# Kernel optimization log

Hardware: AMD Instinct MI355X
Metric: run time of the kernel (lower is better)

The kernel has to match this reference:

```python
import jax, jax.numpy as jnp
import numpy as np

N = 100000
E = 1600000
F_IN = 128
HID = 128
C = 10
NEG_SLOPE = 0.2


def setup_inputs() -> dict:
    key = jax.random.key(0)
    ks = jax.random.split(key, 12)
    x = jax.random.normal(ks[0], (N, F_IN), dtype=jnp.float32)
    edge_index = jax.random.randint(ks[1], (2, E), 0, N, dtype=jnp.int64)
    batch = jnp.zeros((N,), dtype=jnp.int64)
    s1 = 1.0 / np.sqrt(F_IN)
    s2 = 1.0 / np.sqrt(HID)
    return {
        "x": x,
        "edge_index": edge_index,
        "batch": batch,
        "W1": jax.random.normal(ks[2], (F_IN, HID), dtype=jnp.float32) * s1,
        "a_src1": jax.random.normal(ks[3], (HID,), dtype=jnp.float32) * s2,
        "a_dst1": jax.random.normal(ks[4], (HID,), dtype=jnp.float32) * s2,
        "b1": jnp.zeros((HID,), dtype=jnp.float32),
        "W2": jax.random.normal(ks[5], (HID, HID), dtype=jnp.float32) * s2,
        "a_src2": jax.random.normal(ks[6], (HID,), dtype=jnp.float32) * s2,
        "a_dst2": jax.random.normal(ks[7], (HID,), dtype=jnp.float32) * s2,
        "b2": jnp.zeros((HID,), dtype=jnp.float32),
        "Wlin": jax.random.normal(ks[8], (HID, C), dtype=jnp.float32) * s2,
        "blin": jnp.zeros((C,), dtype=jnp.float32),
    }


def gat_conv(x, src, dst, W, a_src, a_dst, b):
    # PyG GATConv, heads=1: h = xW; alpha_e = softmax_dst(leaky_relu(a_src.h[src] + a_dst.h[dst]))
    h = x @ W                                  # [N, H]
    alpha_s = h @ a_src                        # [N]
    alpha_d = h @ a_dst                        # [N]
    e = jax.nn.leaky_relu(alpha_s[src] + alpha_d[dst], NEG_SLOPE)  # [E]
    m = jax.ops.segment_max(e, dst, num_segments=N)                # per-dst max (stable softmax)
    ex = jnp.exp(e - m[dst])
    denom = jax.ops.segment_sum(ex, dst, num_segments=N)
    alpha = ex / (denom[dst] + 1e-16)          # [E]
    out = jax.ops.segment_sum(h[src] * alpha[:, None], dst, num_segments=N)
    return out + b


def reference(x, edge_index, batch, W1, a_src1, a_dst1, b1, W2, a_src2, a_dst2, b2, Wlin, blin):
    x = x.astype(jnp.float32)
    loops = jnp.arange(N, dtype=edge_index.dtype)
    src = jnp.concatenate([edge_index[0], loops])  # add_self_loops=True
    dst = jnp.concatenate([edge_index[1], loops])
    h = jax.nn.relu(gat_conv(x, src, dst, W1, a_src1, a_dst1, b1))
    h = jax.nn.relu(gat_conv(h, src, dst, W2, a_src2, a_dst2, b2))
    # dropout(p=0.5) is identity in eval mode
    return h @ Wlin + blin
```

## Files before the change

### kernel.cpp

```cpp
#include <hip/hip_runtime.h>

#define N_NODES 100000
#define N_EDGES 1600000
#define TOTE    (N_EDGES + N_NODES)
#define NEG     0.2f
#define NB      ((N_NODES + 255) >> 8)
#define BCAP    5120
#define BINBLK  391

typedef __attribute__((ext_vector_type(8))) short bf16x8;
typedef __attribute__((ext_vector_type(4))) float floatx4;

__device__ __forceinline__ unsigned short f2bf(float f) {
  unsigned int u = __float_as_uint(f);
  u += 0x7fffu + ((u >> 16) & 1u);
  return (unsigned short)(u >> 16);
}
__device__ __forceinline__ float bf_lo(unsigned int r) { return __uint_as_float(r << 16); }
__device__ __forceinline__ float bf_hi(unsigned int r) { return __uint_as_float(r & 0xffff0000u); }

__global__ __launch_bounds__(256) void k_wprep(const float* __restrict__ W1, const float* __restrict__ W2,
                                               unsigned short* __restrict__ B1hi, unsigned short* __restrict__ B1lo,
                                               unsigned short* __restrict__ B2hi, unsigned short* __restrict__ B2lo,
                                               int* __restrict__ bucketCnt) {
  int b = blockIdx.x;
  int t = threadIdx.x;
  if (b == 16) {
    for (int i = t; i < NB * 16; i += 256) bucketCnt[i] = 0;
    return;
  }
  const float* W = (b < 8) ? W1 : W2;
  unsigned short* Bh = (b < 8) ? B1hi : B2hi;
  unsigned short* Bl = (b < 8) ? B1lo : B2lo;
  int ntile = b & 7;
  int kq = t >> 6, lane = t & 63;
  int q = lane >> 4, m = lane & 15;
  int n = ntile * 16 + m;
  union { unsigned short us[8]; uint4 u4; } hi, lo;
#pragma unroll
  for (int j = 0; j < 8; ++j) {
    int k = kq * 32 + q * 8 + j;
    float w = W[(size_t)k * 128 + n];
    unsigned int u = __float_as_uint(w);
    hi.us[j] = (unsigned short)(u >> 16);
    float res = w - __uint_as_float(u & 0xffff0000u);
    lo.us[j] = f2bf(res);
  }
  size_t fo = ((size_t)(ntile * 4 + kq) * 64 + lane) * 8;
  *reinterpret_cast<uint4*>(Bh + fo) = hi.u4;
  *reinterpret_cast<uint4*>(Bl + fo) = lo.u4;
}

__global__ __launch_bounds__(256, 4) void k_binA_gemm1(
    const int* __restrict__ ei, int* __restrict__ bucketCnt, unsigned int* __restrict__ binned,
    const float* __restrict__ x,
    const unsigned short* __restrict__ Bhi, const unsigned short* __restrict__ Blo,
    unsigned short* __restrict__ Cb,
    const float* __restrict__ avS, const float* __restrict__ avD,
    float* __restrict__ aS, float* __restrict__ aD,
    float* __restrict__ slotS, float* __restrict__ slotD) {
  __shared__ union {
    struct { int hist[NB]; int cur[NB]; } a;
    struct { char sbuf[64 * 528]; float redS[256]; float redD[256];
             float mS[64]; float mD[64]; } g;
  } sm;
  int t = threadIdx.x;

  if (blockIdx.x < BINBLK) {
    for (int b = t; b < NB; b += 256) sm.a.hist[b] = 0;
    __syncthreads();
    unsigned int pk[16]; int bk[16];
#pragma unroll
    for (int j = 0; j < 16; ++j) {
      int idx = blockIdx.x * 4096 + j * 256 + t;
      if (idx < N_EDGES) {
        int s = ei[idx], d = ei[N_EDGES + idx];
        bk[j] = d >> 8;
        pk[j] = ((unsigned int)s << 8) | (unsigned int)(d & 255);
        atomicAdd(&sm.a.hist[bk[j]], 1);
      } else bk[j] = -1;
    }
    __syncthreads();
    for (int b = t; b < NB; b += 256) {
      int h = sm.a.hist[b];
      if (h) sm.a.cur[b] = b * BCAP + atomicAdd(&bucketCnt[b * 16], h);
    }
    __syncthreads();
#pragma unroll
    for (int j = 0; j < 16; ++j) {
      if (bk[j] >= 0) {
        int pos = atomicAdd(&sm.a.cur[bk[j]], 1);
        binned[pos] = pk[j];
      }
    }
    return;
  }

  int bid = blockIdx.x - BINBLK;
  int w = t >> 6, lane = t & 63;
  int q = lane >> 4, m = lane & 15;
  int rbase = bid * 64;
  const char* Ab = (const char*)x;

  for (int c = w; c < 33; c += 4) {
    int L = c * 1024 + lane * 16;
    int r = L / 528;
    int off = L - r * 528;
    int gr = min(rbase + r, N_NODES - 1);
    const char* src = (off < 512) ? (Ab + (size_t)gr * 512 + off) : Ab;
    __builtin_amdgcn_global_load_lds((const __attribute__((address_space(1))) void*)src,
                                     (__attribute__((address_space(3))) void*)(sm.g.sbuf + c * 1024),
                                     16, 0, 0);
  }

  floatx4 acc[4][2];
#pragma unroll
  for (int mt = 0; mt < 4; ++mt)
#pragma unroll
    for (int nt = 0; nt < 2; ++nt) acc[mt][nt] = (floatx4){0.f, 0.f, 0.f, 0.f};

  __syncthreads();

#pragma unroll
  for (int k0 = 0; k0 < 4; ++k0) {
    bf16x8 Bh[2], Bl[2], Ah[4], Al[4];
#pragma unroll
    for (int nt = 0; nt < 2; ++nt) {
      int ntg = w * 2 + nt;
      size_t fo = ((size_t)(ntg * 4 + k0) * 64 + lane) * 8;
      Bh[nt] = *reinterpret_cast<const bf16x8*>(Bhi + fo);
      Bl[nt] = *reinterpret_cast<const bf16x8*>(Blo + fo);
    }
#pragma unroll
    for (int mt = 0; mt < 4; ++mt) {
      int R = mt * 16 + m;
      const char* ap = sm.g.sbuf + R * 528 + k0 * 128 + q * 32;
      float4 v0 = *reinterpret_cast<const float4*>(ap);
      float4 v1 = *reinterpret_cast<const float4*>(ap + 16);
      float av[8] = {v0.x, v0.y, v0.z, v0.w, v1.x, v1.y, v1.z, v1.w};
      union { unsigned short us[8]; bf16x8 v; } uh, ul;
#pragma unroll
      for (int j = 0; j < 8; ++j) {
        unsigned int u = __float_as_uint(av[j]);
        uh.us[j] = (unsigned short)(u >> 16);
        float res = av[j] - __uint_as_float(u & 0xffff0000u);
        ul.us[j] = f2bf(res);
      }
      Ah[mt] = uh.v; Al[mt] = ul.v;
    }
#pragma unroll
    for (int mt = 0; mt < 4; ++mt)
#pragma unroll
      for (int nt = 0; nt < 2; ++nt) {
        acc[mt][nt] = __builtin_amdgcn_mfma_f32_16x16x32_bf16(Ah[mt], Bh[nt], acc[mt][nt], 0, 0, 0);
        acc[mt][nt] = __builtin_amdgcn_mfma_f32_16x16x32_bf16(Ah[mt], Bl[nt], acc[mt][nt], 0, 0, 0);
        acc[mt][nt] = __builtin_amdgcn_mfma_f32_16x16x32_bf16(Al[mt], Bh[nt], acc[mt][nt], 0, 0, 0);
      }
  }

  float avs[2], avd[2];
#pragma unroll
  for (int nt = 0; nt < 2; ++nt) {
    int c = w * 32 + nt * 16 + m;
    avs[nt] = avS[c];
    avd[nt] = avD[c];
  }
#pragma unroll
  for (int mt = 0; mt < 4; ++mt)
#pragma unroll
    for (int r = 0; r < 4; ++r) {
      float ps = acc[mt][0][r] * avs[0] + acc[mt][1][r] * avs[1];
      float pd = acc[mt][0][r] * avd[0] + acc[mt][1][r] * avd[1];
      ps += __shfl_xor(ps, 1); pd += __shfl_xor(pd, 1);
      ps += __shfl_xor(ps, 2); pd += __shfl_xor(pd, 2);
      ps += __shfl_xor(ps, 4); pd += __shfl_xor(pd, 4);
      ps += __shfl_xor(ps, 8); pd += __shfl_xor(pd, 8);
      if (m == 0) {
        int rl = mt * 16 + q * 4 + r;
        sm.g.redS[rl * 4 + w] = ps;
        sm.g.redD[rl * 4 + w] = pd;
      }
    }

  __syncthreads();
  unsigned short* sC = (unsigned short*)sm.g.sbuf;

#pragma unroll
  for (int mt = 0; mt < 4; ++mt)
#pragma unroll
    for (int nt = 0; nt < 2; ++nt)
#pragma unroll
      for (int r = 0; r < 4; ++r) {
        int rl = mt * 16 + q * 4 + r;
        int cl = w * 32 + nt * 16 + m;
        sC[rl * 136 + cl] = f2bf(acc[mt][nt][r]);
      }
  __syncthreads();

#pragma unroll
  for (int i = 0; i < 4; ++i) {
    int idx = i * 256 + t;
    int rl = idx >> 4, kk = idx & 15;
    int gr = rbase + rl;
    if (gr < N_NODES)
      *reinterpret_cast<uint4*>(Cb + (size_t)gr * 128 + kk * 8) =
          *reinterpret_cast<const uint4*>(sC + rl * 136 + kk * 8);
  }

  if (t < 64) {
    int gr = rbase + t;
    bool ok = gr < N_NODES;
    float ps = sm.g.redS[t * 4] + sm.g.redS[t * 4 + 1] + sm.g.redS[t * 4 + 2] + sm.g.redS[t * 4 + 3];
    float pd = sm.g.redD[t * 4] + sm.g.redD[t * 4 + 1] + sm.g.redD[t * 4 + 2] + sm.g.redD[t * 4 + 3];
    if (ok) { aS[gr] = ps; aD[gr] = pd; }
    sm.g.mS[t] = ok ? ps : -1e30f;
    sm.g.mD[t] = ok ? pd : -1e30f;
  }
  __syncthreads();
#pragma unroll
  for (int off = 32; off > 0; off >>= 1) {
    if (t < off) {
      sm.g.mS[t] = fmaxf(sm.g.mS[t], sm.g.mS[t + off]);
      sm.g.mD[t] = fmaxf(sm.g.mD[t], sm.g.mD[t + off]);
    }
    __syncthreads();
  }
  if (t == 0) { slotS[bid] = sm.g.mS[0]; slotD[bid] = sm.g.mD[0]; }
}

__global__ __launch_bounds__(512) void k_bin_scan(const int* __restrict__ bucketCnt,
                                                  int* __restrict__ binOffs) {
  __shared__ int sc[512];
  int t = threadIdx.x;
  int v = (t < NB) ? bucketCnt[t * 16] : 0;
  sc[t] = v; __syncthreads();
  for (int off = 1; off < 512; off <<= 1) {
    int x = (t >= off) ? sc[t - off] : 0;
    __syncthreads();
    sc[t] += x;
    __syncthreads();
  }
  int excl = sc[t] - v;
  if (t <= NB) binOffs[t] = excl;
}

__global__ __launch_bounds__(256) void k_binB(const unsigned int* __restrict__ binned,
                                              const int* __restrict__ binOffs,
                                              int* __restrict__ offs, int* __restrict__ srcs) {
  __shared__ int cnt[256];
  __shared__ int sc[256];
  __shared__ int cur[256];
  int b = blockIdx.x;
  int t = threadIdx.x;
  int node0 = b << 8;
  int nNodes = min(256, N_NODES - node0);
  int cntE = binOffs[b + 1] - binOffs[b];
  int e0 = b * BCAP, e1 = e0 + cntE;
  int base = binOffs[b] + node0;

  cnt[t] = 0; __syncthreads();
  for (int i = e0 + t; i < e1; i += 256) atomicAdd(&cnt[binned[i] & 255u], 1);
  __syncthreads();

  int v = (t < nNodes) ? cnt[t] + 1 : 0;
  sc[t] = v; __syncthreads();
  for (int off = 1; off < 256; off <<= 1) {
    int x = (t >= off) ? sc[t - off] : 0;
    __syncthreads();
    sc[t] += x;
    __syncthreads();
  }
  int excl = sc[t] - v;
  if (t < nNodes) {
    offs[node0 + t] = base + excl;
    srcs[base + excl] = node0 + t;
  }
  cur[t] = excl + 1;
  __syncthreads();

  for (int i = e0 + t; i < e1; i += 256) {
    unsigned int e = binned[i];
    int j = (int)(e & 255u);
    int s = (int)(e >> 8);
    int p = atomicAdd(&cur[j], 1);
    srcs[base + p] = s;
  }
  if (b == 0 && t == 0) offs[N_NODES] = TOTE;
}

template <bool SPLIT>
__global__ __launch_bounds__(256, 4) void k_gemm_mfma(const void* __restrict__ Aptr,
                                                   const unsigned short* __restrict__ Bhi,
                                                   const unsigned short* __restrict__ Blo,
                                                   unsigned short* __restrict__ Cb,
                                                   const float* __restrict__ avS, const float* __restrict__ avD,
                                                   float* __restrict__ aS, float* __restrict__ aD,
                                                   float* __restrict__ slotS, float* __restrict__ slotD) {
  constexpr int SRCB  = SPLIT ? 512 : 256;
  constexpr int ROWB  = SPLIT ? 528 : 272;
  constexpr int ABYTES = 64 * ROWB;
  constexpr int CHUNKS = ABYTES / 1024;
  __shared__ char sbuf[ABYTES];
  __shared__ float redS[64 * 4], redD[64 * 4];
  __shared__ float mS[64], mD[64];
  int t = threadIdx.x;
  int w = t >> 6, lane = t & 63;
  int q = lane >> 4, m = lane & 15;
  int rbase = blockIdx.x * 64;
  const char* Ab = (const char*)Aptr;

  for (int c = w; c < CHUNKS; c += 4) {
    int L = c * 1024 + lane * 16;
    int r = L / ROWB;
    int off = L - r * ROWB;
    int gr = min(rbase + r, N_NODES - 1);
    const char* src = (off < SRCB) ? (Ab + (size_t)gr * SRCB + off) : Ab;
    __builtin_amdgcn_global_load_lds((const __attribute__((address_space(1))) void*)src,
                                     (__attribute__((address_space(3))) void*)(sbuf + c * 1024),
                                     16, 0, 0);
  }

  floatx4 acc[4][2];
#pragma unroll
  for (int mt = 0; mt < 4; ++mt)
#pragma unroll
    for (int nt = 0; nt < 2; ++nt) acc[mt][nt] = (floatx4){0.f, 0.f, 0.f, 0.f};

  __syncthreads();

#pragma unroll
  for (int k0 = 0; k0 < 4; ++k0) {
    bf16x8 Bh[2], Bl[2], Ah[4], Al[4];
#pragma unroll
    for (int nt = 0; nt < 2; ++nt) {
      int ntg = w * 2 + nt;
      size_t fo = ((size_t)(ntg * 4 + k0) * 64 + lane) * 8;
      Bh[nt] = *reinterpret_cast<const bf16x8*>(Bhi + fo);
      Bl[nt] = *reinterpret_cast<const bf16x8*>(Blo + fo);
    }
#pragma unroll
    for (int mt = 0; mt < 4; ++mt) {
      int R = mt * 16 + m;
      if constexpr (SPLIT) {
        const char* ap = sbuf + R * ROWB + k0 * 128 + q * 32;
        float4 v0 = *reinterpret_cast<const float4*>(ap);
        float4 v1 = *reinterpret_cast<const float4*>(ap + 16);
        float av[8] = {v0.x, v0.y, v0.z, v0.w, v1.x, v1.y, v1.z, v1.w};
        union { unsigned short us[8]; bf16x8 v; } uh, ul;
#pragma unroll
        for (int j = 0; j < 8; ++j) {
          unsigned int u = __float_as_uint(av[j]);
          uh.us[j] = (unsigned short)(u >> 16);
          float res = av[j] - __uint_as_float(u & 0xffff0000u);
          ul.us[j] = f2bf(res);
        }
        Ah[mt] = uh.v; Al[mt] = ul.v;
      } else {
        Ah[mt] = *reinterpret_cast<const bf16x8*>(sbuf + R * ROWB + k0 * 64 + q * 16);
      }
    }
#pragma unroll
    for (int mt = 0; mt < 4; ++mt)
#pragma unroll
      for (int nt = 0; nt < 2; ++nt) {
        acc[mt][nt] = __builtin_amdgcn_mfma_f32_16x16x32_bf16(Ah[mt], Bh[nt], acc[mt][nt], 0, 0, 0);
        acc[mt][nt] = __builtin_amdgcn_mfma_f32_16x16x32_bf16(Ah[mt], Bl[nt], acc[mt][nt], 0, 0, 0);
        if constexpr (SPLIT)
          acc[mt][nt] = __builtin_amdgcn_mfma_f32_16x16x32_bf16(Al[mt], Bh[nt], acc[mt][nt], 0, 0, 0);
      }
  }

  float avs[2], avd[2];
#pragma unroll
  for (int nt = 0; nt < 2; ++nt) {
    int c = w * 32 + nt * 16 + m;
    avs[nt] = avS[c];
    avd[nt] = avD[c];
  }
#pragma unroll
  for (int mt = 0; mt < 4; ++mt)
#pragma unroll
    for (int r = 0; r < 4; ++r) {
      float ps = acc[mt][0][r] * avs[0] + acc[mt][1][r] * avs[1];
      float pd = acc[mt][0][r] * avd[0] + acc[mt][1][r] * avd[1];
      ps += __shfl_xor(ps, 1); pd += __shfl_xor(pd, 1);
      ps += __shfl_xor(ps, 2); pd += __shfl_xor(pd, 2);
      ps += __shfl_xor(ps, 4); pd += __shfl_xor(pd, 4);
      ps += __shfl_xor(ps, 8); pd += __shfl_xor(pd, 8);
      if (m == 0) {
        int rl = mt * 16 + q * 4 + r;
        redS[rl * 4 + w] = ps;
        redD[rl * 4 + w] = pd;
      }
    }

  __syncthreads();
  unsigned short* sC = (unsigned short*)sbuf;

#pragma unroll
  for (int mt = 0; mt < 4; ++mt)
#pragma unroll
    for (int nt = 0; nt < 2; ++nt)
#pragma unroll
      for (int r = 0; r < 4; ++r) {
        int rl = mt * 16 + q * 4 + r;
        int cl = w * 32 + nt * 16 + m;
        sC[rl * 136 + cl] = f2bf(acc[mt][nt][r]);
      }
  __syncthreads();

#pragma unroll
  for (int i = 0; i < 4; ++i) {
    int idx = i * 256 + t;
    int rl = idx >> 4, kk = idx & 15;
    int gr = rbase + rl;
    if (gr < N_NODES)
      *reinterpret_cast<uint4*>(Cb + (size_t)gr * 128 + kk * 8) =
          *reinterpret_cast<const uint4*>(sC + rl * 136 + kk * 8);
  }

  if (t < 64) {
    int gr = rbase + t;
    bool ok = gr < N_NODES;
    float ps = redS[t * 4] + redS[t * 4 + 1] + redS[t * 4 + 2] + redS[t * 4 + 3];
    float pd = redD[t * 4] + redD[t * 4 + 1] + redD[t * 4 + 2] + redD[t * 4 + 3];
    if (ok) { aS[gr] = ps; aD[gr] = pd; }
    mS[t] = ok ? ps : -1e30f;
    mD[t] = ok ? pd : -1e30f;
  }
  __syncthreads();
#pragma unroll
  for (int off = 32; off > 0; off >>= 1) {
    if (t < off) { mS[t] = fmaxf(mS[t], mS[t + off]); mD[t] = fmaxf(mD[t], mD[t + off]); }
    __syncthreads();
  }
  if (t == 0) { slotS[blockIdx.x] = mS[0]; slotD[blockIdx.x] = mD[0]; }
}

__global__ __launch_bounds__(256) void k_gmax(const float* __restrict__ slotS,
                                              const float* __restrict__ slotD,
                                              int n, float* __restrict__ gMh) {
  __shared__ float sS[256], sD[256];
  int t = threadIdx.x;
  float ms = -1e30f, md = -1e30f;
  for (int i = t; i < n; i += 256) { ms = fmaxf(ms, slotS[i]); md = fmaxf(md, slotD[i]); }
  sS[t] = ms; sD[t] = md;
  __syncthreads();
#pragma unroll
  for (int off = 128; off > 0; off >>= 1) {
    if (t < off) { sS[t] = fmaxf(sS[t], sS[t + off]); sD[t] = fmaxf(sD[t], sD[t + off]); }
    __syncthreads();
  }
  if (t == 0) {
    float M = sS[0] + sD[0];
    gMh[0] = (M > 0.f) ? M : NEG * M;
  }
}

#define FMA8(E, R)                                     \
  do {                                                 \
    acc[0] += (E) * bf_lo((R).x); acc[1] += (E) * bf_hi((R).x); \
    acc[2] += (E) * bf_lo((R).y); acc[3] += (E) * bf_hi((R).y); \
    acc[4] += (E) * bf_lo((R).z); acc[5] += (E) * bf_hi((R).z); \
    acc[6] += (E) * bf_lo((R).w); acc[7] += (E) * bf_hi((R).w); \
  } while (0)

#define LDG(R0, R1, R2, R3, E0, E1, E2, E3, J)                                                   \
  do {                                                                                           \
    float2 q0 = pairs[pbase + (J) + 0];                                                          \
    float2 q1 = pairs[pbase + (J) + 1];                                                          \
    float2 q2 = pairs[pbase + (J) + 2];                                                          \
    float2 q3 = pairs[pbase + (J) + 3];                                                          \
    E0 = q0.x; E1 = q1.x; E2 = q2.x; E3 = q3.x;                                                  \
    R0 = *reinterpret_cast<const uint4*>(hbl + ((size_t)(unsigned)__float_as_int(q0.y) << 7));   \
    R1 = *reinterpret_cast<const uint4*>(hbl + ((size_t)(unsigned)__float_as_int(q1.y) << 7));   \
    R2 = *reinterpret_cast<const uint4*>(hbl + ((size_t)(unsigned)__float_as_int(q2.y) << 7));   \
    R3 = *reinterpret_cast<const uint4*>(hbl + ((size_t)(unsigned)__float_as_int(q3.y) << 7));   \
  } while (0)
#define FMAG(R0, R1, R2, R3, E0, E1, E2, E3) \
  do { FMA8(E0, R0); FMA8(E1, R1); FMA8(E2, R2); FMA8(E3, R3); } while (0)

template <bool FINAL>
__global__ __launch_bounds__(256) void k_aggregate(const unsigned short* __restrict__ hb,
                                                   const float* __restrict__ aS,
                                                   const float* __restrict__ aD,
                                                   const int* __restrict__ offs,
                                                   const int* __restrict__ srcs,
                                                   const float* __restrict__ bias,
                                                   const float* __restrict__ gMh,
                                                   unsigned short* __restrict__ outb,
                                                   const float* __restrict__ Wl,
                                                   const float* __restrict__ bl,
                                                   float* __restrict__ out) {
  __shared__ float2 pairs[16 * 17];
  __shared__ float sWt[FINAL ? 10 * 144 : 1];
  __shared__ float sbl[FINAL ? 16 : 1];
  int t = threadIdx.x;
  if constexpr (FINAL) {
    if (t < 128) {
      int jj = t >> 5, ii = t & 31;
#pragma unroll
      for (int c = 0; c < 10; ++c) sWt[c * 144 + jj * 36 + ii] = Wl[t * 10 + c];
    }
    if (t < 10) sbl[t] = bl[t];
    __syncthreads();
  }
  int g = t >> 4;
  int l = t & 15;
  int dst = blockIdx.x * 16 + g;
  float Mh = gMh[0];
  int beg = offs[dst], end = offs[dst + 1];
  float adn = aD[dst];
  float denom = 0.f;
  float acc[8];
#pragma unroll
  for (int k = 0; k < 8; ++k) acc[k] = 0.f;
  const int pbase = g * 17;
  const unsigned short* hbl = hb + l * 8;

  uint4 ra0, ra1, ra2, ra3, rb0, rb1, rb2, rb3;
  float ea0, ea1, ea2, ea3, eb0, eb1, eb2, eb3;

  for (int chunk = beg; chunk < end; chunk += 16) {
    int i = chunk + l;
    float ex = 0.f; int s = 0;
    if (i < end) {
      s = srcs[i];
      float e = aS[s] + adn;
      e = (e > 0.f) ? e : NEG * e;
      ex = __expf(e - Mh);
    }
    denom += ex;
    pairs[pbase + l] = make_float2(ex, __int_as_float(s));
    int cnt = end - chunk; if (cnt > 16) cnt = 16;
    LDG(ra0, ra1, ra2, ra3, ea0, ea1, ea2, ea3, 0);
    int j = 0;
    for (;;) {
      bool more = (j + 4) < cnt;
      if (more) LDG(rb0, rb1, rb2, rb3, eb0, eb1, eb2, eb3, j + 4);
      FMAG(ra0, ra1, ra2, ra3, ea0, ea1, ea2, ea3);
      j += 4;
      if (!more) break;
      bool more2 = (j + 4) < cnt;
      if (more2) LDG(ra0, ra1, ra2, ra3, ea0, ea1, ea2, ea3, j + 4);
      FMAG(rb0, rb1, rb2, rb3, eb0, eb1, eb2, eb3);
      j += 4;
      if (!more2) break;
    }
  }

  denom += __shfl_xor(denom, 1);
  denom += __shfl_xor(denom, 2);
  denom += __shfl_xor(denom, 4);
  denom += __shfl_xor(denom, 8);
  float inv = 1.f / (denom + 1e-16f);
  float4 b0 = *reinterpret_cast<const float4*>(bias + l * 8);
  float4 b1 = *reinterpret_cast<const float4*>(bias + l * 8 + 4);
  float o0 = fmaxf(acc[0] * inv + b0.x, 0.f), o1 = fmaxf(acc[1] * inv + b0.y, 0.f);
  float o2 = fmaxf(acc[2] * inv + b0.z, 0.f), o3 = fmaxf(acc[3] * inv + b0.w, 0.f);
  float o4 = fmaxf(acc[4] * inv + b1.x, 0.f), o5 = fmaxf(acc[5] * inv + b1.y, 0.f);
  float o6 = fmaxf(acc[6] * inv + b1.z, 0.f), o7 = fmaxf(acc[7] * inv + b1.w, 0.f);

  if constexpr (!FINAL) {
    union { unsigned short us[8]; uint4 u4; } oo;
    oo.us[0] = f2bf(o0); oo.us[1] = f2bf(o1); oo.us[2] = f2bf(o2); oo.us[3] = f2bf(o3);
    oo.us[4] = f2bf(o4); oo.us[5] = f2bf(o5); oo.us[6] = f2bf(o6); oo.us[7] = f2bf(o7);
    *reinterpret_cast<uint4*>(outb + (size_t)dst * 128 + l * 8) = oo.u4;
  } else {
    float p[10];
#pragma unroll
    for (int c = 0; c < 10; ++c) {
      const float4* wp = reinterpret_cast<const float4*>(&sWt[c * 144 + (l >> 2) * 36 + (l & 3) * 8]);
      float4 w0 = wp[0], w1 = wp[1];
      p[c] = o0 * w0.x + o1 * w0.y + o2 * w0.z + o3 * w0.w +
             o4 * w1.x + o5 * w1.y + o6 * w1.z + o7 * w1.w;
    }
#pragma unroll
    for (int c = 0; c < 10; ++c) {
      p[c] += __shfl_xor(p[c], 1);
      p[c] += __shfl_xor(p[c], 2);
      p[c] += __shfl_xor(p[c], 4);
      p[c] += __shfl_xor(p[c], 8);
    }
    if (l == 0) {
      float* orow = out + (size_t)dst * 10;
      *reinterpret_cast<float2*>(orow + 0) = make_float2(p[0] + sbl[0], p[1] + sbl[1]);
      *reinterpret_cast<float2*>(orow + 2) = make_float2(p[2] + sbl[2], p[3] + sbl[3]);
      *reinterpret_cast<float2*>(orow + 4) = make_float2(p[4] + sbl[4], p[5] + sbl[5]);
      *reinterpret_cast<float2*>(orow + 6) = make_float2(p[6] + sbl[6], p[7] + sbl[7]);
      *reinterpret_cast<float2*>(orow + 8) = make_float2(p[8] + sbl[8], p[9] + sbl[9]);
    }
  }
}

extern "C" void kernel_launch(void* const* d_in, const int* in_sizes, int n_in,
                              void* d_out, int out_size, void* d_ws, size_t ws_size,
                              hipStream_t stream) {
  const float* x   = (const float*)d_in[0];
  const int*   ei  = (const int*)d_in[1];
  const float* W1  = (const float*)d_in[3];
  const float* as1 = (const float*)d_in[4];
  const float* ad1 = (const float*)d_in[5];
  const float* b1  = (const float*)d_in[6];
  const float* W2  = (const float*)d_in[7];
  const float* as2 = (const float*)d_in[8];
  const float* ad2 = (const float*)d_in[9];
  const float* b2  = (const float*)d_in[10];
  const float* Wl  = (const float*)d_in[11];
  const float* bl  = (const float*)d_in[12];
  float* out = (float*)d_out;

  char* p = (char*)d_ws;
  unsigned short* hb   = (unsigned short*)p; p += (size_t)N_NODES * 128 * sizeof(unsigned short);
  unsigned short* hagg = (unsigned short*)p; p += (size_t)N_NODES * 128 * sizeof(unsigned short);
  float* aS    = (float*)p; p += (size_t)N_NODES * sizeof(float);
  float* aD    = (float*)p; p += (size_t)N_NODES * sizeof(float);
  int* offs    = (int*)p;   p += (size_t)(N_NODES + 4) * sizeof(int);
  int* srcs    = (int*)p;   p += (size_t)TOTE * sizeof(int);
  int* bucketCnt = (int*)p; p += (size_t)NB * 16 * sizeof(int);
  int* binOffs   = (int*)p; p += (size_t)(NB + 4) * sizeof(int);
  float* slotS = (float*)p; p += 2048 * sizeof(float);
  float* slotD = (float*)p; p += 2048 * sizeof(float);
  float* gMh = (float*)p;   p += 4 * sizeof(float);
  unsigned short* B1hi = (unsigned short*)p; p += 128 * 128 * sizeof(unsigned short);
  unsigned short* B1lo = (unsigned short*)p; p += 128 * 128 * sizeof(unsigned short);
  unsigned short* B2hi = (unsigned short*)p; p += 128 * 128 * sizeof(unsigned short);
  unsigned short* B2lo = (unsigned short*)p; p += 128 * 128 * sizeof(unsigned short);
  unsigned int* binned = (unsigned int*)hagg;

  int gemmBlocks = (N_NODES + 63) / 64;
  int aggBlocks  = N_NODES / 16;

  k_wprep<<<17, 256, 0, stream>>>(W1, W2, B1hi, B1lo, B2hi, B2lo, bucketCnt);
  k_binA_gemm1<<<BINBLK + gemmBlocks, 256, 0, stream>>>(ei, bucketCnt, binned,
                                                        x, B1hi, B1lo, hb, as1, ad1,
                                                        aS, aD, slotS, slotD);
  k_bin_scan<<<1, 512, 0, stream>>>(bucketCnt, binOffs);
  k_binB<<<NB, 256, 0, stream>>>(binned, binOffs, offs, srcs);
  k_gmax<<<1, 256, 0, stream>>>(slotS, slotD, gemmBlocks, gMh);
  k_aggregate<false><<<aggBlocks, 256, 0, stream>>>(hb, aS, aD, offs, srcs, b1, gMh, hagg,
                                                    nullptr, nullptr, nullptr);
  k_gemm_mfma<false><<<gemmBlocks, 256, 0, stream>>>(hagg, B2hi, B2lo, hb, as2, ad2, aS, aD, slotS, slotD);
  k_gmax<<<1, 256, 0, stream>>>(slotS, slotD, gemmBlocks, gMh);
  k_aggregate<true><<<aggBlocks, 256, 0, stream>>>(hb, aS, aD, offs, srcs, b2, gMh, hagg,
                                                   Wl, bl, out);
}
```

Measured before the change: 325.1 us.

## Split layer-1 GEMM across both binning kernels to overlap with bin phases

The first-layer feature GEMM blocks are split in half. One half still runs alongside the edge-binning pass A, and the other half now runs inside a new fused kernel alongside binning pass B, which replaces the standalone k_binB. This balances work between the two launches so GEMM blocks fill the GPU while the latency-bound binning blocks run. The cost is a larger shared-memory footprint for the binning blocks in pass B, which shares a union with the GEMM buffers and may lower occupancy.

```diff
diff --git a/kernel.cpp b/kernel.cpp
--- a/kernel.cpp
+++ b/kernel.cpp
@@ -7,6 +7,8 @@
 #define NB      ((N_NODES + 255) >> 8)
 #define BCAP    5120
 #define BINBLK  391
+#define G1H1    782
+#define G1H2    781
 
 typedef __attribute__((ext_vector_type(8))) short bf16x8;
 typedef __attribute__((ext_vector_type(4))) float floatx4;
@@ -49,6 +51,142 @@
   size_t fo = ((size_t)(ntile * 4 + kq) * 64 + lane) * 8;
   *reinterpret_cast<uint4*>(Bh + fo) = hi.u4;
   *reinterpret_cast<uint4*>(Bl + fo) = lo.u4;
+}
+
+__device__ __forceinline__ void gemm1_body(
+    int bid, int t, char* sbuf, float* redS, float* redD, float* mS, float* mD,
+    const float* __restrict__ x,
+    const unsigned short* __restrict__ Bhi, const unsigned short* __restrict__ Blo,
+    unsigned short* __restrict__ Cb,
+    const float* __restrict__ avS, const float* __restrict__ avD,
+    float* __restrict__ aS, float* __restrict__ aD,
+    float* __restrict__ slotS, float* __restrict__ slotD) {
+  int w = t >> 6, lane = t & 63;
+  int q = lane >> 4, m = lane & 15;
+  int rbase = bid * 64;
+  const char* Ab = (const char*)x;
+
+  for (int c = w; c < 33; c += 4) {
+    int L = c * 1024 + lane * 16;
+    int r = L / 528;
+    int off = L - r * 528;
+    int gr = min(rbase + r, N_NODES - 1);
+    const char* src = (off < 512) ? (Ab + (size_t)gr * 512 + off) : Ab;
+    __builtin_amdgcn_global_load_lds((const __attribute__((address_space(1))) void*)src,
+                                     (__attribute__((address_space(3))) void*)(sbuf + c * 1024),
+                                     16, 0, 0);
+  }
+
+  floatx4 acc[4][2];
+#pragma unroll
+  for (int mt = 0; mt < 4; ++mt)
+#pragma unroll
+    for (int nt = 0; nt < 2; ++nt) acc[mt][nt] = (floatx4){0.f, 0.f, 0.f, 0.f};
+
+  __syncthreads();
+
+#pragma unroll
+  for (int k0 = 0; k0 < 4; ++k0) {
+    bf16x8 Bh[2], Bl[2], Ah[4], Al[4];
+#pragma unroll
+    for (int nt = 0; nt < 2; ++nt) {
+      int ntg = w * 2 + nt;
+      size_t fo = ((size_t)(ntg * 4 + k0) * 64 + lane) * 8;
+      Bh[nt] = *reinterpret_cast<const bf16x8*>(Bhi + fo);
+      Bl[nt] = *reinterpret_cast<const bf16x8*>(Blo + fo);
+    }
+#pragma unroll
+    for (int mt = 0; mt < 4; ++mt) {
+      int R = mt * 16 + m;
+      const char* ap = sbuf + R * 528 + k0 * 128 + q * 32;
+      float4 v0 = *reinterpret_cast<const float4*>(ap);
+      float4 v1 = *reinterpret_cast<const float4*>(ap + 16);
+      float av[8] = {v0.x, v0.y, v0.z, v0.w, v1.x, v1.y, v1.z, v1.w};
+      union { unsigned short us[8]; bf16x8 v; } uh, ul;
+#pragma unroll
+      for (int j = 0; j < 8; ++j) {
+        unsigned int u = __float_as_uint(av[j]);
+        uh.us[j] = (unsigned short)(u >> 16);
+        float res = av[j] - __uint_as_float(u & 0xffff0000u);
+        ul.us[j] = f2bf(res);
+      }
+      Ah[mt] = uh.v; Al[mt] = ul.v;
+    }
+#pragma unroll
+    for (int mt = 0; mt < 4; ++mt)
+#pragma unroll
+      for (int nt = 0; nt < 2; ++nt) {
+        acc[mt][nt] = __builtin_amdgcn_mfma_f32_16x16x32_bf16(Ah[mt], Bh[nt], acc[mt][nt], 0, 0, 0);
+        acc[mt][nt] = __builtin_amdgcn_mfma_f32_16x16x32_bf16(Ah[mt], Bl[nt], acc[mt][nt], 0, 0, 0);
+        acc[mt][nt] = __builtin_amdgcn_mfma_f32_16x16x32_bf16(Al[mt], Bh[nt], acc[mt][nt], 0, 0, 0);
+      }
+  }
+
+  float avs[2], avd[2];
+#pragma unroll
+  for (int nt = 0; nt < 2; ++nt) {
+    int c = w * 32 + nt * 16 + m;
+    avs[nt] = avS[c];
+    avd[nt] = avD[c];
+  }
+#pragma unroll
+  for (int mt = 0; mt < 4; ++mt)
+#pragma unroll
+    for (int r = 0; r < 4; ++r) {
+      float ps = acc[mt][0][r] * avs[0] + acc[mt][1][r] * avs[1];
+      float pd = acc[mt][0][r] * avd[0] + acc[mt][1][r] * avd[1];
+      ps += __shfl_xor(ps, 1); pd += __shfl_xor(pd, 1);
+      ps += __shfl_xor(ps, 2); pd += __shfl_xor(pd, 2);
+      ps += __shfl_xor(ps, 4); pd += __shfl_xor(pd, 4);
+      ps += __shfl_xor(ps, 8); pd += __shfl_xor(pd, 8);
+      if (m == 0) {
+        int rl = mt * 16 + q * 4 + r;
+        redS[rl * 4 + w] = ps;
+        redD[rl * 4 + w] = pd;
+      }
+    }
+
+  __syncthreads();
+  unsigned short* sC = (unsigned short*)sbuf;
+
+#pragma unroll
+  for (int mt = 0; mt < 4; ++mt)
+#pragma unroll
+    for (int nt = 0; nt < 2; ++nt)
+#pragma unroll
+      for (int r = 0; r < 4; ++r) {
+        int rl = mt * 16 + q * 4 + r;
+        int cl = w * 32 + nt * 16 + m;
+        sC[rl * 136 + cl] = f2bf(acc[mt][nt][r]);
+      }
+  __syncthreads();
+
+#pragma unroll
+  for (int i = 0; i < 4; ++i) {
+    int idx = i * 256 + t;
+    int rl = idx >> 4, kk = idx & 15;
+    int gr = rbase + rl;
+    if (gr < N_NODES)
+      *reinterpret_cast<uint4*>(Cb + (size_t)gr * 128 + kk * 8) =
+          *reinterpret_cast<const uint4*>(sC + rl * 136 + kk * 8);
+  }
+
+  if (t < 64) {
+    int gr = rbase + t;
+    bool ok = gr < N_NODES;
+    float ps = redS[t * 4] + redS[t * 4 + 1] + redS[t * 4 + 2] + redS[t * 4 + 3];
+    float pd = redD[t * 4] + redD[t * 4 + 1] + redD[t * 4 + 2] + redD[t * 4 + 3];
+    if (ok) { aS[gr] = ps; aD[gr] = pd; }
+    mS[t] = ok ? ps : -1e30f;
+    mD[t] = ok ? pd : -1e30f;
+  }
+  __syncthreads();
+#pragma unroll
+  for (int off = 32; off > 0; off >>= 1) {
+    if (t < off) { mS[t] = fmaxf(mS[t], mS[t + off]); mD[t] = fmaxf(mD[t], mD[t + off]); }
+    __syncthreads();
+  }
+  if (t == 0) { slotS[bid] = mS[0]; slotD[bid] = mD[0]; }
 }
 
 __global__ __launch_bounds__(256, 4) void k_binA_gemm1(
@@ -96,136 +234,67 @@
     return;
   }
 
-  int bid = blockIdx.x - BINBLK;
-  int w = t >> 6, lane = t & 63;
-  int q = lane >> 4, m = lane & 15;
-  int rbase = bid * 64;
-  const char* Ab = (const char*)x;
-
-  for (int c = w; c < 33; c += 4) {
-    int L = c * 1024 + lane * 16;
-    int r = L / 528;
-    int off = L - r * 528;
-    int gr = min(rbase + r, N_NODES - 1);
-    const char* src = (off < 512) ? (Ab + (size_t)gr * 512 + off) : Ab;
-    __builtin_amdgcn_global_load_lds((const __attribute__((address_space(1))) void*)src,
-                                     (__attribute__((address_space(3))) void*)(sm.g.sbuf + c * 1024),
-                                     16, 0, 0);
-  }
-
-  floatx4 acc[4][2];
-#pragma unroll
-  for (int mt = 0; mt < 4; ++mt)
-#pragma unroll
-    for (int nt = 0; nt < 2; ++nt) acc[mt][nt] = (floatx4){0.f, 0.f, 0.f, 0.f};
-
-  __syncthreads();
-
-#pragma unroll
-  for (int k0 = 0; k0 < 4; ++k0) {
-    bf16x8 Bh[2], Bl[2], Ah[4], Al[4];
-#pragma unroll
-    for (int nt = 0; nt < 2; ++nt) {
-      int ntg = w * 2 + nt;
-      size_t fo = ((size_t)(ntg * 4 + k0) * 64 + lane) * 8;
-      Bh[nt] = *reinterpret_cast<const bf16x8*>(Bhi + fo);
-      Bl[nt] = *reinterpret_cast<const bf16x8*>(Blo + fo);
-    }
-#pragma unroll
-    for (int mt = 0; mt < 4; ++mt) {
-      int R = mt * 16 + m;
-      const char* ap = sm.g.sbuf + R * 528 + k0 * 128 + q * 32;
-      float4 v0 = *reinterpret_cast<const float4*>(ap);
-      float4 v1 = *reinterpret_cast<const float4*>(ap + 16);
-      float av[8] = {v0.x, v0.y, v0.z, v0.w, v1.x, v1.y, v1.z, v1.w};
-      union { unsigned short us[8]; bf16x8 v; } uh, ul;
-#pragma unroll
-      for (int j = 0; j < 8; ++j) {
-        unsigned int u = __float_as_uint(av[j]);
-        uh.us[j] = (unsigned short)(u >> 16);
-        float res = av[j] - __uint_as_float(u & 0xffff0000u);
-        ul.us[j] = f2bf(res);
-      }
-      Ah[mt] = uh.v; Al[mt] = ul.v;
-    }
-#pragma unroll
-    for (int mt = 0; mt < 4; ++mt)
-#pragma unroll
-      for (int nt = 0; nt < 2; ++nt) {
-        acc[mt][nt] = __builtin_amdgcn_mfma_f32_16x16x32_bf16(Ah[mt], Bh[nt], acc[mt][nt], 0, 0, 0);
-        acc[mt][nt] = __builtin_amdgcn_mfma_f32_16x16x32_bf16(Ah[mt], Bl[nt], acc[mt][nt], 0, 0, 0);
-        acc[mt][nt] = __builtin_amdgcn_mfma_f32_16x16x32_bf16(Al[mt], Bh[nt], acc[mt][nt], 0, 0, 0);
-      }
-  }
-
-  float avs[2], avd[2];
-#pragma unroll
-  for (int nt = 0; nt < 2; ++nt) {
-    int c = w * 32 + nt * 16 + m;
-    avs[nt] = avS[c];
-    avd[nt] = avD[c];
-  }
-#pragma unroll
-  for (int mt = 0; mt < 4; ++mt)
-#pragma unroll
-    for (int r = 0; r < 4; ++r) {
-      float ps = acc[mt][0][r] * avs[0] + acc[mt][1][r] * avs[1];
-      float pd = acc[mt][0][r] * avd[0] + acc[mt][1][r] * avd[1];
-      ps += __shfl_xor(ps, 1); pd += __shfl_xor(pd, 1);
-      ps += __shfl_xor(ps, 2); pd += __shfl_xor(pd, 2);
-      ps += __shfl_xor(ps, 4); pd += __shfl_xor(pd, 4);
-      ps += __shfl_xor(ps, 8); pd += __shfl_xor(pd, 8);
-      if (m == 0) {
-        int rl = mt * 16 + q * 4 + r;
-        sm.g.redS[rl * 4 + w] = ps;
-        sm.g.redD[rl * 4 + w] = pd;
-      }
-    }
-
-  __syncthreads();
-  unsigned short* sC = (unsigned short*)sm.g.sbuf;
-
-#pragma unroll
-  for (int mt = 0; mt < 4; ++mt)
-#pragma unroll
-    for (int nt = 0; nt < 2; ++nt)
-#pragma unroll
-      for (int r = 0; r < 4; ++r) {
-        int rl = mt * 16 + q * 4 + r;
-        int cl = w * 32 + nt * 16 + m;
-        sC[rl * 136 + cl] = f2bf(acc[mt][nt][r]);
-      }
-  __syncthreads();
-
-#pragma unroll
-  for (int i = 0; i < 4; ++i) {
-    int idx = i * 256 + t;
-    int rl = idx >> 4, kk = idx & 15;
-    int gr = rbase + rl;
-    if (gr < N_NODES)
-      *reinterpret_cast<uint4*>(Cb + (size_t)gr * 128 + kk * 8) =
-          *reinterpret_cast<const uint4*>(sC + rl * 136 + kk * 8);
-  }
-
-  if (t < 64) {
-    int gr = rbase + t;
-    bool ok = gr < N_NODES;
-    float ps = sm.g.redS[t * 4] + sm.g.redS[t * 4 + 1] + sm.g.redS[t * 4 + 2] + sm.g.redS[t * 4 + 3];
-    float pd = sm.g.redD[t * 4] + sm.g.redD[t * 4 + 1] + sm.g.redD[t * 4 + 2] + sm.g.redD[t * 4 + 3];
-    if (ok) { aS[gr] = ps; aD[gr] = pd; }
-    sm.g.mS[t] = ok ? ps : -1e30f;
-    sm.g.mD[t] = ok ? pd : -1e30f;
-  }
-  __syncthreads();
-#pragma unroll
-  for (int off = 32; off > 0; off >>= 1) {
-    if (t < off) {
-      sm.g.mS[t] = fmaxf(sm.g.mS[t], sm.g.mS[t + off]);
-      sm.g.mD[t] = fmaxf(sm.g.mD[t], sm.g.mD[t + off]);
-    }
-    __syncthreads();
-  }
-  if (t == 0) { slotS[bid] = sm.g.mS[0]; slotD[bid] = sm.g.mD[0]; }
+  gemm1_body(blockIdx.x - BINBLK, t, sm.g.sbuf, sm.g.redS, sm.g.redD, sm.g.mS, sm.g.mD,
+             x, Bhi, Blo, Cb, avS, avD, aS, aD, slotS, slotD);
+}
+
+__global__ __launch_bounds__(256, 4) void k_binB_gemm1(
+    const unsigned int* __restrict__ binned, const int* __restrict__ binOffs,
+    int* __restrict__ offs, int* __restrict__ srcs,
+    const float* __restrict__ x,
+    const unsigned short* __restrict__ Bhi, const unsigned short* __restrict__ Blo,
+    unsigned short* __restrict__ Cb,
+    const float* __restrict__ avS, const float* __restrict__ avD,
+    float* __restrict__ aS, float* __restrict__ aD,
+    float* __restrict__ slotS, float* __restrict__ slotD) {
+  __shared__ union {
+    struct { int cnt[256]; int sc[256]; int cur[256]; } b;
+    struct { char sbuf[64 * 528]; float redS[256]; float redD[256];
+             float mS[64]; float mD[64]; } g;
+  } sm;
+  int t = threadIdx.x;
+
+  if (blockIdx.x < BINBLK) {
+    int b = blockIdx.x;
+    int node0 = b << 8;
+    int nNodes = min(256, N_NODES - node0);
+    int cntE = binOffs[b + 1] - binOffs[b];
+    int e0 = b * BCAP, e1 = e0 + cntE;
+    int base = binOffs[b] + node0;
+
+    sm.b.cnt[t] = 0; __syncthreads();
+    for (int i = e0 + t; i < e1; i += 256) atomicAdd(&sm.b.cnt[binned[i] & 255u], 1);
+    __syncthreads();
+
+    int v = (t < nNodes) ? sm.b.cnt[t] + 1 : 0;
+    sm.b.sc[t] = v; __syncthreads();
+    for (int off = 1; off < 256; off <<= 1) {
+      int x2 = (t >= off) ? sm.b.sc[t - off] : 0;
+      __syncthreads();
+      sm.b.sc[t] += x2;
+      __syncthreads();
+    }
+    int excl = sm.b.sc[t] - v;
+    if (t < nNodes) {
+      offs[node0 + t] = base + excl;
+      srcs[base + excl] = node0 + t;
+    }
+    sm.b.cur[t] = excl + 1;
+    __syncthreads();
+
+    for (int i = e0 + t; i < e1; i += 256) {
+      unsigned int e = binned[i];
+      int j = (int)(e & 255u);
+      int s = (int)(e >> 8);
+      int p = atomicAdd(&sm.b.cur[j], 1);
+      srcs[base + p] = s;
+    }
+    if (b == 0 && t == 0) offs[N_NODES] = TOTE;
+    return;
+  }
+
+  gemm1_body(G1H1 + (blockIdx.x - BINBLK), t, sm.g.sbuf, sm.g.redS, sm.g.redD, sm.g.mS, sm.g.mD,
+             x, Bhi, Blo, Cb, avS, avD, aS, aD, slotS, slotD);
 }
 
 __global__ __launch_bounds__(512) void k_bin_scan(const int* __restrict__ bucketCnt,
@@ -242,50 +311,6 @@
   }
   int excl = sc[t] - v;
   if (t <= NB) binOffs[t] = excl;
-}
-
-__global__ __launch_bounds__(256) void k_binB(const unsigned int* __restrict__ binned,
-                                              const int* __restrict__ binOffs,
-                                              int* __restrict__ offs, int* __restrict__ srcs) {
-  __shared__ int cnt[256];
-  __shared__ int sc[256];
-  __shared__ int cur[256];
-  int b = blockIdx.x;
-  int t = threadIdx.x;
-  int node0 = b << 8;
-  int nNodes = min(256, N_NODES - node0);
-  int cntE = binOffs[b + 1] - binOffs[b];
-  int e0 = b * BCAP, e1 = e0 + cntE;
-  int base = binOffs[b] + node0;
-
-  cnt[t] = 0; __syncthreads();
-  for (int i = e0 + t; i < e1; i += 256) atomicAdd(&cnt[binned[i] & 255u], 1);
-  __syncthreads();
-
-  int v = (t < nNodes) ? cnt[t] + 1 : 0;
-  sc[t] = v; __syncthreads();
-  for (int off = 1; off < 256; off <<= 1) {
-    int x = (t >= off) ? sc[t - off] : 0;
-    __syncthreads();
-    sc[t] += x;
-    __syncthreads();
-  }
-  int excl = sc[t] - v;
-  if (t < nNodes) {
-    offs[node0 + t] = base + excl;
-    srcs[base + excl] = node0 + t;
-  }
-  cur[t] = excl + 1;
-  __syncthreads();
-
-  for (int i = e0 + t; i < e1; i += 256) {
-    unsigned int e = binned[i];
-    int j = (int)(e & 255u);
-    int s = (int)(e >> 8);
-    int p = atomicAdd(&cur[j], 1);
-    srcs[base + p] = s;
-  }
-  if (b == 0 && t == 0) offs[N_NODES] = TOTE;
 }
 
 template <bool SPLIT>
@@ -632,11 +657,13 @@
   int aggBlocks  = N_NODES / 16;
 
   k_wprep<<<17, 256, 0, stream>>>(W1, W2, B1hi, B1lo, B2hi, B2lo, bucketCnt);
-  k_binA_gemm1<<<BINBLK + gemmBlocks, 256, 0, stream>>>(ei, bucketCnt, binned,
-                                                        x, B1hi, B1lo, hb, as1, ad1,
-                                                        aS, aD, slotS, slotD);
+  k_binA_gemm1<<<BINBLK + G1H1, 256, 0, stream>>>(ei, bucketCnt, binned,
+                                                  x, B1hi, B1lo, hb, as1, ad1,
+                                                  aS, aD, slotS, slotD);
   k_bin_scan<<<1, 512, 0, stream>>>(bucketCnt, binOffs);
-  k_binB<<<NB, 256, 0, stream>>>(binned, binOffs, offs, srcs);
+  k_binB_gemm1<<<BINBLK + G1H2, 256, 0, stream>>>(binned, binOffs, offs, srcs,
+                                                  x, B1hi, B1lo, hb, as1, ad1,
+                                                  aS, aD, slotS, slotD);
   k_gmax<<<1, 256, 0, stream>>>(slotS, slotD, gemmBlocks, gMh);
   k_aggregate<false><<<aggBlocks, 256, 0, stream>>>(hb, aS, aD, offs, srcs, b1, gMh, hagg,
                                                     nullptr, nullptr, nullptr);
```

Measured after the change: 326.3 us. Within noise of the previous version (+0.4%).
